# Kernel optimization log

Measured on AMD Instinct MI355X. Metric: run time of the kernel, lower is better.

The kernel has to match this reference:

```python
import jax, jax.numpy as jnp
import numpy as np

ALPHA, GAMMA, EPS = 0.25, 2.0, 1e-05
MU, BINS, MMT = 0.02, 10, 0.7  # GHMR_Loss defaults


def focal_loss(x, y):
    # forward() calls focal_loss without a mask (source bug); mask == 1 everywhere.
    x_t = x * (2.0 * y - 1.0) + (1.0 - y)
    alpha_t = ALPHA * (2.0 * y - 1.0) + (1.0 - y)
    return jnp.sum(-alpha_t * (1.0 - x_t) ** GAMMA * jnp.log(x_t + EPS))


def ghmr_loss(inp, tgt, mask):
    c = inp.shape[-1]
    inp = inp.reshape(-1, c)
    tgt = tgt.reshape(-1, c)
    diff = inp - tgt
    loss = jnp.sqrt(diff * diff + MU * MU) - MU  # ASL1 loss
    g = jax.lax.stop_gradient(jnp.abs(diff) / jnp.sqrt(MU * MU + diff * diff))  # in [0,1)
    valid = mask.reshape(-1, 1) > 0.1                       # [N,1] bool
    valid_b = jnp.broadcast_to(valid, g.shape)              # [N,C]
    tot = jnp.maximum(jnp.sum(valid.astype(jnp.float32)), 1.0)
    # edges are uniform [i/bins, (i+1)/bins), last edge extended to 1000 -> floor binning
    bin_idx = jnp.minimum((g * BINS).astype(jnp.int32), BINS - 1)
    counts = jax.ops.segment_sum(valid_b.astype(jnp.float32).ravel(),
                                 bin_idx.ravel(), num_segments=BINS)
    acc_sum = (1.0 - MMT) * counts                          # momentum EMA from zero-init state
    n = jnp.sum(counts > 0).astype(jnp.float32)
    w_per_bin = jnp.where(counts > 0, tot / jnp.maximum(acc_sum, 1e-30), 0.0)
    weights = jnp.where(valid_b, w_per_bin[bin_idx], 0.0)
    weights = jnp.where(n > 0, weights / jnp.maximum(n, 1.0), weights)
    return jnp.sum(loss * weights) / tot


def setup_inputs() -> dict:
    key = jax.random.key(0)
    k1, k2, k3, k4 = jax.random.split(key, 4)
    B, H, W = 32, 400, 352
    cls_t = (jax.random.uniform(k1, (B, H, W, 1)) < 0.3).astype(jnp.float32)  # binary objectness
    loc_t = jax.random.normal(k2, (B, H, W, 7), dtype=jnp.float32)
    cls_p = jax.random.uniform(k3, (B, H, W, 1), dtype=jnp.float32)           # prob-like preds
    loc_p = loc_t + 0.03 * jax.random.normal(k4, (B, H, W, 7), dtype=jnp.float32)  # spread g over bins
    preds = jnp.concatenate([cls_p, loc_p], axis=-1)
    targets = jnp.concatenate([cls_t, loc_t], axis=-1)
    return {"preds": preds, "targets": targets}


def reference(preds, targets):
    B, H, W = targets.shape[0], targets.shape[1], targets.shape[2]
    cls_preds, loc_preds = preds[..., 0:1], preds[..., 1:]
    cls_targets, loc_targets = targets[..., 0:1], targets[..., 1:]
    cls_loss = focal_loss(cls_preds, cls_targets) / (B * H * W)
    reg_loss = ghmr_loss(loc_preds, loc_targets, cls_targets)
    return (cls_loss + reg_loss,
            jax.lax.stop_gradient(reg_loss),
            jax.lax.stop_gradient(cls_loss))
```

## Files before the change

kernel.cpp:

```cpp
#include <hip/hip_runtime.h>


#define NQ 22

typedef float vf4 __attribute__((ext_vector_type(4)));

__device__ __forceinline__ float wave_sum(float v) {
    v += __shfl_down(v, 32);
    v += __shfl_down(v, 16);
    v += __shfl_down(v, 8);
    v += __shfl_down(v, 4);
    v += __shfl_down(v, 2);
    v += __shfl_down(v, 1);
    return v;
}

__device__ __forceinline__ void ghm_epilogue(float lac[10], float facc,
                                             unsigned vcnt, const unsigned cnt[10],
                                             float* __restrict__ part, int nb) {
    const int tid = threadIdx.x;
    float vq[11] = { lac[0], lac[1], lac[2], lac[3], lac[4],
                     lac[5], lac[6], lac[7], lac[8], lac[9], facc };
#pragma unroll
    for (int q = 0; q < 11; ++q) vq[q] = wave_sum(vq[q]);

    __shared__ float sm[4][NQ];
    const int wave = tid >> 6, lane = tid & 63;
    if (lane == 0) {
#pragma unroll
        for (int q = 0; q < 11; ++q) sm[wave][q] = vq[q];
        sm[wave][11] = (float)vcnt;
        sm[wave][12] = 0.f;
#pragma unroll
        for (int b = 1; b < 10; ++b) sm[wave][12 + b] = (float)cnt[b];
    }
    __syncthreads();
    if (tid < NQ) {
        float v = sm[0][tid] + sm[1][tid] + sm[2][tid] + sm[3][tid];
        part[(size_t)tid * nb + blockIdx.x] = v;
    }
}

__global__ __launch_bounds__(256)
void ghm_pass1_c4(const vf4* __restrict__ preds, const vf4* __restrict__ tgts,
                  int n_pix, float* __restrict__ part, int nb) {
    constexpr float MU2 = 4.0e-4f;
    const float C[10] = { -0.5f,
                          4.0404041e-6f, 1.6666667e-5f, 3.9560441e-5f,
                          7.6190476e-5f, 1.3333333e-4f, 2.2500000e-4f,
                          3.8431373e-4f, 7.1111111e-4f, 1.7052632e-3f };

    float lac[10];
#pragma unroll
    for (int b = 0; b < 10; ++b) lac[b] = 0.f;
    float facc = 0.f;
    unsigned int cnt[10] = {0,0,0,0,0,0,0,0,0,0};
    unsigned int vcnt = 0;

    const int tid = threadIdx.x;

    for (long g = (long)blockIdx.x * 256 + tid; 4 * g < (long)n_pix;
         g += (long)gridDim.x * 256) {
        const long b4 = 8 * g;
        vf4 p[8], t[8];
#pragma unroll
        for (int j = 0; j < 8; ++j) p[j] = preds[b4 + j];
#pragma unroll
        for (int j = 0; j < 8; ++j) t[j] = tgts[b4 + j];

        bool vld[4];
#pragma unroll
        for (int i = 0; i < 4; ++i) {
            vld[i] = t[2 * i].x > 0.1f;
            float x  = p[2 * i].x;
            float xt = vld[i] ? x : 1.f - x;
            float at = vld[i] ? 0.25f : 0.75f;
            float om = 1.f - xt;
            facc += -at * om * om * __logf(xt + 1e-5f);
            vcnt += (unsigned)__builtin_popcountll(__ballot(vld[i]));
        }

#pragma unroll
        for (int i = 0; i < 4; ++i) {
            float pd[7] = { p[2*i].y, p[2*i].z, p[2*i].w,
                            p[2*i+1].x, p[2*i+1].y, p[2*i+1].z, p[2*i+1].w };
            float td[7] = { t[2*i].y, t[2*i].z, t[2*i].w,
                            t[2*i+1].x, t[2*i+1].y, t[2*i+1].z, t[2*i+1].w };
            const bool m = vld[i];
#pragma unroll
            for (int e = 0; e < 7; ++e) {
                float d  = pd[e] - td[e];
                float d2 = d * d;
                float s  = __builtin_amdgcn_sqrtf(__builtin_fmaf(d, d, MU2));
                float loss = s - 0.02f;
                lac[0] += m ? loss : 0.f;
                float d2m = m ? d2 : -1.f;
#pragma unroll
                for (int b = 1; b < 10; ++b) {
                    bool pb = d2m >= C[b];
                    lac[b] += pb ? loss : 0.f;
                    cnt[b] += (unsigned)__builtin_popcountll(__ballot(pb));
                }
            }
        }
    }
    ghm_epilogue(lac, facc, vcnt, cnt, part, nb);
}

__global__ __launch_bounds__(256)
void ghm_pass1_g2(const vf4* __restrict__ preds, const vf4* __restrict__ tgts,
                  int n_pix, float* __restrict__ part, int nb) {
    constexpr float MU2 = 4.0e-4f;
    const float C[10] = { -0.5f,
                          4.0404041e-6f, 1.6666667e-5f, 3.9560441e-5f,
                          7.6190476e-5f, 1.3333333e-4f, 2.2500000e-4f,
                          3.8431373e-4f, 7.1111111e-4f, 1.7052632e-3f };

    float lac[10];
#pragma unroll
    for (int b = 0; b < 10; ++b) lac[b] = 0.f;
    float facc = 0.f;
    unsigned int cnt[10] = {0,0,0,0,0,0,0,0,0,0};
    unsigned int vcnt = 0;

    const int tid = threadIdx.x;
    const long total4 = 2L * (long)n_pix;

    for (long g = (long)blockIdx.x * 256 + tid; 2 * g < (long)n_pix;
         g += (long)gridDim.x * 256) {
        const long b4 = 4 * g;
        const bool in1 = (2 * g + 1) < (long)n_pix;
        const long i1 = (b4 + 1 < total4) ? b4 + 1 : total4 - 1;
        const long i2 = (b4 + 2 < total4) ? b4 + 2 : total4 - 1;
        const long i3 = (b4 + 3 < total4) ? b4 + 3 : total4 - 1;

        vf4 pA = preds[b4], pB = preds[i1], pC = preds[i2], pD = preds[i3];
        vf4 tA = tgts[b4],  tB = tgts[i1],  tC = tgts[i2],  tD = tgts[i3];

        bool v1 = tA.x > 0.1f;
        bool v2 = in1 && (tC.x > 0.1f);
        {
            float x = pA.x;
            float xt = v1 ? x : 1.f - x;
            float at = v1 ? 0.25f : 0.75f;
            float om = 1.f - xt;
            facc += -at * om * om * __logf(xt + 1e-5f);
        }
        {
            bool vv = tC.x > 0.1f;
            float x = pC.x;
            float xt = vv ? x : 1.f - x;
            float at = vv ? 0.25f : 0.75f;
            float om = 1.f - xt;
            float f = -at * om * om * __logf(xt + 1e-5f);
            facc += in1 ? f : 0.f;
        }
        vcnt += (unsigned)__builtin_popcountll(__ballot(v1));
        vcnt += (unsigned)__builtin_popcountll(__ballot(v2));

        float pd[14] = {pA.y,pA.z,pA.w, pB.x,pB.y,pB.z,pB.w,
                        pC.y,pC.z,pC.w, pD.x,pD.y,pD.z,pD.w};
        float td[14] = {tA.y,tA.z,tA.w, tB.x,tB.y,tB.z,tB.w,
                        tC.y,tC.z,tC.w, tD.x,tD.y,tD.z,tD.w};
#pragma unroll
        for (int e = 0; e < 14; ++e) {
            bool m   = (e < 7) ? v1 : v2;
            float d  = pd[e] - td[e];
            float d2 = d * d;
            float s  = __builtin_amdgcn_sqrtf(__builtin_fmaf(d, d, MU2));
            float loss = s - 0.02f;
            lac[0] += m ? loss : 0.f;
            float d2m = m ? d2 : -1.f;
#pragma unroll
            for (int b = 1; b < 10; ++b) {
                bool pb = d2m >= C[b];
                lac[b] += pb ? loss : 0.f;
                cnt[b] += (unsigned)__builtin_popcountll(__ballot(pb));
            }
        }
    }
    ghm_epilogue(lac, facc, vcnt, cnt, part, nb);
}

__global__ __launch_bounds__(256)
void ghm_pass2(const float* __restrict__ part, int nb, float* __restrict__ red) {
    const int q = blockIdx.x;
    const int tid = threadIdx.x;
    float v = 0.f;
    for (int i = tid; i < nb; i += 256) v += part[(size_t)q * nb + i];
    v = wave_sum(v);
    __shared__ float wv[4];
    if ((tid & 63) == 0) wv[tid >> 6] = v;
    __syncthreads();
    if (tid == 0) red[q] = wv[0] + wv[1] + wv[2] + wv[3];
}

__global__ __launch_bounds__(64)
void ghm_pass3(const float* __restrict__ red, float* __restrict__ out,
               float inv_npix) {
    if (threadIdx.x == 0) {
        float tot = fmaxf(red[11], 1.f);
        float c0  = 7.f * red[11];
        float n = 0.f, sum = 0.f;
#pragma unroll
        for (int b = 0; b < 10; ++b) {
            float ccb = (b == 0) ? c0 : red[12 + b];
            float cb  = ccb    - (b < 9 ? red[12 + b + 1] : 0.f);
            float lb  = red[b] - (b < 9 ? red[b + 1]      : 0.f);
            if (cb > 0.f) {
                n += 1.f;
                sum += tot / fmaxf(0.3f * cb, 1e-30f) * lb;
            }
        }
        float reg = sum / fmaxf(n, 1.f) / tot;
        float cls = red[10] * inv_npix;
        out[0] = cls + reg;
        out[1] = reg;
        out[2] = cls;
    }
}

extern "C" void kernel_launch(void* const* d_in, const int* in_sizes, int n_in,
                              void* d_out, int out_size, void* d_ws, size_t ws_size,
                              hipStream_t stream) {
    const float* preds = (const float*)d_in[0];
    const float* tgts  = (const float*)d_in[1];
    const int n_pix = in_sizes[0] / 8;

    const bool clean = (n_pix % 1024) == 0;
    long want_nb = clean ? (long)n_pix / 1024 : ((long)n_pix + 511) / 512;
    long cap = ((long)(ws_size / sizeof(float)) - NQ) / NQ;
    long nb_l = want_nb < cap ? want_nb : cap;
    if (nb_l < 1) nb_l = 1;
    int nb = (int)nb_l;

    float* part = (float*)d_ws;
    float* red  = part + (size_t)NQ * nb;
    if (clean)
        ghm_pass1_c4<<<nb, 256, 0, stream>>>((const vf4*)preds, (const vf4*)tgts,
                                             n_pix, part, nb);
    else
        ghm_pass1_g2<<<nb, 256, 0, stream>>>((const vf4*)preds, (const vf4*)tgts,
                                             n_pix, part, nb);
    ghm_pass2<<<NQ, 256, 0, stream>>>(part, nb, red);
    ghm_pass3<<<1, 64, 0, stream>>>(red, (float*)d_out, 1.f / (float)n_pix);
}
```

Measured before the change: 63.54 us.

## Process 8 pixels per thread with double-buffered register loads in clean path

The clean-path kernel now gives each thread a fixed chunk of 8 pixels, processed 2 at a time. The next pair's loads are issued before the current pair is computed, a software double-buffer in registers. Grid size is halved (n_pix/2048 blocks), which cuts partial-sum traffic and epilogue work and hides memory latency behind compute. The cost is higher register pressure and fewer resident waves, and the clean path now also requires n_pix divisible by 2048 and nb within workspace capacity.

New measurement: 229.6 us. 3.61x slower.

```diff
diff --git a/kernel.cpp b/kernel.cpp
--- a/kernel.cpp
+++ b/kernel.cpp
@@ -41,15 +41,60 @@
     }
 }
 
+__device__ __forceinline__ void do2px(vf4 P0, vf4 P1, vf4 P2, vf4 P3,
+                                      vf4 T0, vf4 T1, vf4 T2, vf4 T3,
+                                      float lac[10], float& facc,
+                                      unsigned cnt[10], unsigned& vcnt,
+                                      const float C[10]) {
+    constexpr float MU2 = 4.0e-4f;
+    bool v1 = T0.x > 0.1f;
+    bool v2 = T2.x > 0.1f;
+    {
+        float x  = P0.x;
+        float xt = v1 ? x : 1.f - x;
+        float at = v1 ? 0.25f : 0.75f;
+        float om = 1.f - xt;
+        facc += -at * om * om * __logf(xt + 1e-5f);
+    }
+    {
+        float x  = P2.x;
+        float xt = v2 ? x : 1.f - x;
+        float at = v2 ? 0.25f : 0.75f;
+        float om = 1.f - xt;
+        facc += -at * om * om * __logf(xt + 1e-5f);
+    }
+    vcnt += (unsigned)__builtin_popcountll(__ballot(v1));
+    vcnt += (unsigned)__builtin_popcountll(__ballot(v2));
+
+    float pd[14] = {P0.y,P0.z,P0.w, P1.x,P1.y,P1.z,P1.w,
+                    P2.y,P2.z,P2.w, P3.x,P3.y,P3.z,P3.w};
+    float td[14] = {T0.y,T0.z,T0.w, T1.x,T1.y,T1.z,T1.w,
+                    T2.y,T2.z,T2.w, T3.x,T3.y,T3.z,T3.w};
+#pragma unroll
+    for (int e = 0; e < 14; ++e) {
+        bool  m  = (e < 7) ? v1 : v2;
+        float d  = pd[e] - td[e];
+        float d2 = d * d;
+        float s  = __builtin_amdgcn_sqrtf(__builtin_fmaf(d, d, MU2));
+        float loss = s - 0.02f;
+        lac[0] += m ? loss : 0.f;
+        float d2m = m ? d2 : -1.f;
+#pragma unroll
+        for (int b = 1; b < 10; ++b) {
+            bool pb = d2m >= C[b];
+            lac[b] += pb ? loss : 0.f;
+            cnt[b] += (unsigned)__builtin_popcountll(__ballot(pb));
+        }
+    }
+}
+
 __global__ __launch_bounds__(256)
-void ghm_pass1_c4(const vf4* __restrict__ preds, const vf4* __restrict__ tgts,
+void ghm_pass1_p8(const vf4* __restrict__ preds, const vf4* __restrict__ tgts,
                   int n_pix, float* __restrict__ part, int nb) {
-    constexpr float MU2 = 4.0e-4f;
     const float C[10] = { -0.5f,
                           4.0404041e-6f, 1.6666667e-5f, 3.9560441e-5f,
                           7.6190476e-5f, 1.3333333e-4f, 2.2500000e-4f,
                           3.8431373e-4f, 7.1111111e-4f, 1.7052632e-3f };
-
     float lac[10];
 #pragma unroll
     for (int b = 0; b < 10; ++b) lac[b] = 0.f;
@@ -57,65 +102,50 @@
     unsigned int cnt[10] = {0,0,0,0,0,0,0,0,0,0};
     unsigned int vcnt = 0;
 
-    const int tid = threadIdx.x;
-
-    for (long g = (long)blockIdx.x * 256 + tid; 4 * g < (long)n_pix;
-         g += (long)gridDim.x * 256) {
-        const long b4 = 8 * g;
-        vf4 p[8], t[8];
-#pragma unroll
-        for (int j = 0; j < 8; ++j) p[j] = preds[b4 + j];
-#pragma unroll
-        for (int j = 0; j < 8; ++j) t[j] = tgts[b4 + j];
-
-        bool vld[4];
-#pragma unroll
-        for (int i = 0; i < 4; ++i) {
-            vld[i] = t[2 * i].x > 0.1f;
-            float x  = p[2 * i].x;
-            float xt = vld[i] ? x : 1.f - x;
-            float at = vld[i] ? 0.25f : 0.75f;
-            float om = 1.f - xt;
-            facc += -at * om * om * __logf(xt + 1e-5f);
-            vcnt += (unsigned)__builtin_popcountll(__ballot(vld[i]));
-        }
-
-#pragma unroll
-        for (int i = 0; i < 4; ++i) {
-            float pd[7] = { p[2*i].y, p[2*i].z, p[2*i].w,
-                            p[2*i+1].x, p[2*i+1].y, p[2*i+1].z, p[2*i+1].w };
-            float td[7] = { t[2*i].y, t[2*i].z, t[2*i].w,
-                            t[2*i+1].x, t[2*i+1].y, t[2*i+1].z, t[2*i+1].w };
-            const bool m = vld[i];
-#pragma unroll
-            for (int e = 0; e < 7; ++e) {
-                float d  = pd[e] - td[e];
-                float d2 = d * d;
-                float s  = __builtin_amdgcn_sqrtf(__builtin_fmaf(d, d, MU2));
-                float loss = s - 0.02f;
-                lac[0] += m ? loss : 0.f;
-                float d2m = m ? d2 : -1.f;
-#pragma unroll
-                for (int b = 1; b < 10; ++b) {
-                    bool pb = d2m >= C[b];
-                    lac[b] += pb ? loss : 0.f;
-                    cnt[b] += (unsigned)__builtin_popcountll(__ballot(pb));
-                }
-            }
-        }
-    }
+    const long g = (long)blockIdx.x * 256 + threadIdx.x;
+    const vf4* pp = preds + 16 * g;
+    const vf4* tp = tgts  + 16 * g;
+
+    vf4 pb0[4], tb0[4], pb1[4], tb1[4];
+#pragma unroll
+    for (int j = 0; j < 4; ++j) pb0[j] = pp[j];
+#pragma unroll
+    for (int j = 0; j < 4; ++j) tb0[j] = tp[j];
+
+#pragma unroll
+    for (int j = 0; j < 4; ++j) pb1[j] = pp[4 + j];
+#pragma unroll
+    for (int j = 0; j < 4; ++j) tb1[j] = tp[4 + j];
+    do2px(pb0[0],pb0[1],pb0[2],pb0[3], tb0[0],tb0[1],tb0[2],tb0[3],
+          lac, facc, cnt, vcnt, C);
+
+#pragma unroll
+    for (int j = 0; j < 4; ++j) pb0[j] = pp[8 + j];
+#pragma unroll
+    for (int j = 0; j < 4; ++j) tb0[j] = tp[8 + j];
+    do2px(pb1[0],pb1[1],pb1[2],pb1[3], tb1[0],tb1[1],tb1[2],tb1[3],
+          lac, facc, cnt, vcnt, C);
+
+#pragma unroll
+    for (int j = 0; j < 4; ++j) pb1[j] = pp[12 + j];
+#pragma unroll
+    for (int j = 0; j < 4; ++j) tb1[j] = tp[12 + j];
+    do2px(pb0[0],pb0[1],pb0[2],pb0[3], tb0[0],tb0[1],tb0[2],tb0[3],
+          lac, facc, cnt, vcnt, C);
+
+    do2px(pb1[0],pb1[1],pb1[2],pb1[3], tb1[0],tb1[1],tb1[2],tb1[3],
+          lac, facc, cnt, vcnt, C);
+
     ghm_epilogue(lac, facc, vcnt, cnt, part, nb);
 }
 
 __global__ __launch_bounds__(256)
 void ghm_pass1_g2(const vf4* __restrict__ preds, const vf4* __restrict__ tgts,
                   int n_pix, float* __restrict__ part, int nb) {
-    constexpr float MU2 = 4.0e-4f;
     const float C[10] = { -0.5f,
                           4.0404041e-6f, 1.6666667e-5f, 3.9560441e-5f,
                           7.6190476e-5f, 1.3333333e-4f, 2.2500000e-4f,
                           3.8431373e-4f, 7.1111111e-4f, 1.7052632e-3f };
-
     float lac[10];
 #pragma unroll
     for (int b = 0; b < 10; ++b) lac[b] = 0.f;
@@ -162,6 +192,7 @@
                         pC.y,pC.z,pC.w, pD.x,pD.y,pD.z,pD.w};
         float td[14] = {tA.y,tA.z,tA.w, tB.x,tB.y,tB.z,tB.w,
                         tC.y,tC.z,tC.w, tD.x,tD.y,tD.z,tD.w};
+        constexpr float MU2 = 4.0e-4f;
 #pragma unroll
         for (int e = 0; e < 14; ++e) {
             bool m   = (e < 7) ? v1 : v2;
@@ -227,9 +258,10 @@
     const float* tgts  = (const float*)d_in[1];
     const int n_pix = in_sizes[0] / 8;
 
-    const bool clean = (n_pix % 1024) == 0;
-    long want_nb = clean ? (long)n_pix / 1024 : ((long)n_pix + 511) / 512;
     long cap = ((long)(ws_size / sizeof(float)) - NQ) / NQ;
+    const bool clean = (n_pix % 2048) == 0 && (long)n_pix / 2048 <= cap;
+
+    long want_nb = clean ? (long)n_pix / 2048 : ((long)n_pix + 511) / 512;
     long nb_l = want_nb < cap ? want_nb : cap;
     if (nb_l < 1) nb_l = 1;
     int nb = (int)nb_l;
@@ -237,7 +269,7 @@
     float* part = (float*)d_ws;
     float* red  = part + (size_t)NQ * nb;
     if (clean)
-        ghm_pass1_c4<<<nb, 256, 0, stream>>>((const vf4*)preds, (const vf4*)tgts,
+        ghm_pass1_p8<<<nb, 256, 0, stream>>>((const vf4*)preds, (const vf4*)tgts,
                                              n_pix, part, nb);
     else
         ghm_pass1_g2<<<nb, 256, 0, stream>>>((const vf4*)preds, (const vf4*)tgts,
```
